# Kernel optimization log

Measured on AMD Instinct MI355X. Metric: run time of the kernel, lower is better.

## Reference

```python
import jax, jax.numpy as jnp
import numpy as np

B, F, E = 16384, 50, 64          # batch, field_size, embedding_size
V, D = 100000, 512               # feature_size, deep_init_size
H1, H2 = 1024, 512               # deep_layers
BN_EPS = 1e-10


def setup_inputs() -> dict:
    key = jax.random.key(0)
    ks = jax.random.split(key, 14)
    g0 = np.sqrt(6.0 / (D + H1))
    g1 = np.sqrt(6.0 / (H1 + H2))
    go = np.sqrt(5.0 / (D + 1))
    return {
        "feat_index": jax.random.randint(ks[0], (B, F), 0, V),
        "feat_value": jax.random.uniform(ks[1], (B, F), dtype=jnp.float32),
        "feature_embeddings": jax.random.normal(ks[2], (V, E), dtype=jnp.float32) * 0.01,
        "product_linear": jax.random.normal(ks[3], (D, F, E), dtype=jnp.float32) * 0.01,
        "product_bias": jax.random.normal(ks[4], (D,), dtype=jnp.float32),
        "product_quadratic_inner": jax.random.normal(ks[5], (D, F), dtype=jnp.float32) * 0.01,
        "layer_0": jax.random.uniform(ks[6], (D, H1), minval=-g0, maxval=g0, dtype=jnp.float32),
        "bias_0": jax.random.uniform(ks[7], (1, H1), minval=-g0, maxval=g0, dtype=jnp.float32),
        "layer_1": jax.random.uniform(ks[8], (H1, H2), minval=-g1, maxval=g1, dtype=jnp.float32),
        "bias_1": jax.random.uniform(ks[9], (1, H2), minval=-g1, maxval=g1, dtype=jnp.float32),
        "bn_scale": jax.random.normal(ks[10], (1,), dtype=jnp.float32) * 0.01,
        "bn_offset": jax.random.normal(ks[11], (1,), dtype=jnp.float32) * 0.01,
        "output_w": jax.random.uniform(ks[12], (H2, 1), minval=-go, maxval=go, dtype=jnp.float32),
        "output_b": jnp.float32(0.01),
    }


def reference(feat_index, feat_value, feature_embeddings, product_linear,
              product_bias, product_quadratic_inner, layer_0, bias_0,
              layer_1, bias_1, bn_scale, bn_offset, output_w, output_b):
    # embedding lookup scaled by feature values: (B, F, E)
    emb = feature_embeddings[feat_index] * feat_value[..., None]
    # linear product signal: sum over field+embed dims for each of D units
    lz = jnp.einsum('bfe,dfe->bd', emb, product_linear)          # (B, D)
    # inner quadratic signal: field-weighted sum then L2 norm over embed dim
    s = jnp.einsum('bfe,df->bde', emb, product_quadratic_inner)  # (B, D, E)
    lp = jnp.sqrt(jnp.sum(s * s, axis=-1))                       # (B, D)
    y = jax.nn.relu(lz + lp + product_bias)
    # dropout omitted (deterministic eval-mode reference)
    for W, bvec in ((layer_0, bias_0), (layer_1, bias_1)):
        y = y @ W + bvec
        m = jnp.mean(y, axis=0)
        v = jnp.var(y, axis=0)
        y = (y - m) * jax.lax.rsqrt(v + BN_EPS) * bn_scale + bn_offset
        y = jax.nn.relu(y)
    out = y @ output_w + output_b
    return jax.nn.sigmoid(out)
```

## Files before the change

kernel.cpp:

```cpp
#include <hip/hip_runtime.h>

typedef unsigned short u16;
typedef __attribute__((ext_vector_type(8))) short bf16x8v;
typedef __attribute__((ext_vector_type(4))) float f32x4v;

#define B_SZ 16384
#define F_SZ 50
#define E_SZ 64
#define D_SZ 512
#define H1_SZ 1024
#define H2_SZ 512
#define KL 3200
#define KG 1280

__device__ __forceinline__ float b2f(u16 u){
  union { unsigned int i; float f; } v; v.i = ((unsigned int)u) << 16; return v.f;
}
__device__ __forceinline__ u16 f2b(float f){
  union { float f; unsigned int i; } v; v.f = f;
  unsigned int r = v.i + 0x7FFFu + ((v.i >> 16) & 1u);
  return (u16)(r >> 16);
}

__device__ __forceinline__ void gload16(const u16* g, u16* lds_base_uniform){
#if __has_builtin(__builtin_amdgcn_global_load_lds)
  __builtin_amdgcn_global_load_lds(
      (const __attribute__((address_space(1))) unsigned int*)g,
      (__attribute__((address_space(3))) unsigned int*)lds_base_uniform,
      16, 0, 0);
#else
  int lane = threadIdx.x & 63;
  *(uint4*)(lds_base_uniform + lane*8) = *(const uint4*)g;
#endif
}

__device__ __forceinline__ void swz(int id, int nblog2, int &x, int &y){
  int xcd = id & 7, j = id >> 3;
  x = j & ((1 << nblog2) - 1);
  y = ((j >> nblog2) << 3) | xcd;
}

__global__ __launch_bounds__(256) void k_front(
    const int* __restrict__ fidx, const float* __restrict__ fval,
    const float* __restrict__ femb, u16* __restrict__ embT,
    u16* __restrict__ Gp,
    const float* __restrict__ Wl, u16* __restrict__ WlT,
    const float* __restrict__ Pq, u16* __restrict__ pqq,
    const float* __restrict__ w0, u16* __restrict__ w0T,
    const float* __restrict__ w1, u16* __restrict__ w1T,
    const float* __restrict__ pb, const float* __restrict__ b0,
    float* __restrict__ cvec)
{
  __shared__ int   sidx[F_SZ];
  __shared__ float sfv[F_SZ];
  __shared__ __align__(16) u16 tile[64*72];
  __shared__ __align__(16) u16 gbuf[KG];
  const int r = blockIdx.x, t = threadIdx.x;
  if (r < 16384){
    const int b = r;
    const int wave = t >> 6, lane = t & 63, quad = lane >> 4, l16 = lane & 15;
    if (t < F_SZ){ sidx[t] = fidx[b*F_SZ+t]; sfv[t] = fval[b*F_SZ+t]; }
    if (t < 5) gbuf[1275+t] = 0;
    __syncthreads();
    #pragma unroll
    for (int i=0;i<4;i++){
      int k4 = (i*256+t)*4;
      if (k4 < F_SZ*E_SZ){
        int f = k4>>6, e = k4&63;
        float4 v = *(const float4*)&femb[(size_t)sidx[f]*E_SZ + e];
        float s = sfv[f];
        tile[f*72+e+0] = f2b(v.x*s);
        tile[f*72+e+1] = f2b(v.y*s);
        tile[f*72+e+2] = f2b(v.z*s);
        tile[f*72+e+3] = f2b(v.w*s);
      }
    }
    __syncthreads();
    u16* orow = embT + (size_t)b*KL;
    #pragma unroll
    for (int i=0;i<2;i++){
      int k8 = (i*256+t)*8;
      if (k8 < F_SZ*E_SZ){
        int f = k8>>6, e0 = k8&63;
        *(uint4*)&orow[k8] = *(const uint4*)&tile[f*72+e0];
      }
    }
    static const int TM[10] = {0,0,0,0,1,1,1,2,2,3};
    static const int TN[10] = {0,1,2,3,1,2,3,2,3,3};
    for (int ti = wave; ti < 10; ti += 4){
      const int tm = TM[ti], tn = TN[ti];
      f32x4v g = {0.f,0.f,0.f,0.f};
      #pragma unroll
      for (int ks=0;ks<2;ks++){
        bf16x8v af = *(const bf16x8v*)&tile[(tm*16+l16)*72 + (ks*4+quad)*8];
        bf16x8v bf = *(const bf16x8v*)&tile[(tn*16+l16)*72 + (ks*4+quad)*8];
        g = __builtin_amdgcn_mfma_f32_16x16x32_bf16(af, bf, g, 0, 0, 0);
      }
      const int gn = tn*16 + l16;
      #pragma unroll
      for (int rr=0;rr<4;rr++){
        const int gm = tm*16 + quad*4 + rr;
        if (gm < F_SZ && gn < F_SZ && gn >= gm)
          gbuf[gm*F_SZ - ((gm*(gm-1))>>1) + (gn-gm)] = f2b(g[rr]);
      }
    }
    __syncthreads();
    if (t < 160)
      *(uint4*)&Gp[(size_t)b*KG + t*8] = *(const uint4*)&gbuf[t*8];
  } else if (r < 16896){
    const int d = r - 16384;
    #pragma unroll
    for (int i=0;i<4;i++){
      int k4 = (i*256+t)*4;
      if (k4 < KL){
        float4 v = *(const float4*)&Wl[(size_t)d*KL + k4];
        u16* o = &WlT[(size_t)d*KL + k4];
        o[0]=f2b(v.x); o[1]=f2b(v.y); o[2]=f2b(v.z); o[3]=f2b(v.w);
      }
    }
  } else if (r < 17408){
    const int d = r - 16896;
    const float* prow = &Pq[d*F_SZ];
    u16* orow = &pqq[(size_t)d*KG];
    int trif = 0;
    for (int f=0; f<F_SZ; f++){
      int len = F_SZ - f;
      if (t < len)
        orow[trif + t] = f2b(prow[f]*prow[f+t]*(t ? 2.f : 1.f));
      trif += len;
    }
    if (t < 5) orow[1275+t] = 0;
  } else if (r < 19456){
    int idx = (r-17408)*256 + t;
    int k = idx & 511, n = idx >> 9;
    w0T[idx] = f2b(w0[(size_t)k*H1_SZ + n]);
  } else if (r < 21504){
    int idx = (r-19456)*256 + t;
    int k = idx & 1023, n = idx >> 10;
    w1T[idx] = f2b(w1[(size_t)k*H2_SZ + n]);
  } else {
    int rr = r - 21504;
    int h = (rr & 3)*256 + t;
    int d0 = (rr >> 2)*64;
    float acc = (d0 == 0) ? b0[h] : 0.f;
    #pragma unroll 8
    for (int d=0; d<64; d++) acc += pb[d0+d]*w0[(size_t)(d0+d)*H1_SZ + h];
    atomicAdd(&cvec[h], acc);
  }
}


__global__ __launch_bounds__(256, 2) void k_prod(
    const u16* __restrict__ Ae,
    const u16* __restrict__ Bw,
    const u16* __restrict__ Ag,
    const u16* __restrict__ Bq,
    const float* __restrict__ pbias,
    u16* __restrict__ y0)
{
  __shared__ __align__(16) u16 As[128*128];
  __shared__ __align__(16) u16 Bs[128*128];
  const int tid  = threadIdx.x;
  const int wave = tid >> 6, lane = tid & 63;
  const int quad = lane >> 4, l16 = lane & 15;
  int bx, by;  swz(blockIdx.x, 2, bx, by);
  const int n0 = bx * 128, m0 = by * 128;
  const int lr4 = lane >> 4;
  const int cb  = lane & 15;
  const int sw  = (l16 & 7);

  f32x4v acc1[2][8], acc2[2][8];
  #pragma unroll
  for (int i=0;i<2;i++)
    #pragma unroll
    for (int j=0;j<8;j++){
      acc1[i][j] = (f32x4v){0.f,0.f,0.f,0.f};
      acc2[i][j] = (f32x4v){0.f,0.f,0.f,0.f};
    }

  auto run = [&](const u16* Ap, const u16* Bp, int K, f32x4v (&acc)[2][8]){
    for (int k0 = 0; k0 < K; k0 += 128){
      __syncthreads();
      #pragma unroll
      for (int c=0;c<8;c++){
        const int r0 = wave*32 + c*4;
        const int row = r0 + lr4;
        gload16(Ap + (size_t)(m0 + row)*K + k0 + ((cb ^ (row & 7)) << 3), As + r0*128);
      }
      #pragma unroll
      for (int c=0;c<8;c++){
        const int r0 = wave*32 + c*4;
        const int row = r0 + lr4;
        gload16(Bp + (size_t)(n0 + row)*K + k0 + ((cb ^ (row & 7)) << 3), Bs + r0*128);
      }
      __syncthreads();
      #pragma unroll
      for (int ks=0; ks<4; ks++){
        bf16x8v af[2], bfr[8];
        #pragma unroll
        for (int mt=0;mt<2;mt++)
          af[mt] = *(const bf16x8v*)&As[(wave*32+mt*16+l16)*128 + (((ks*4+quad) ^ sw))*8];
        #pragma unroll
        for (int nt=0;nt<8;nt++)
          bfr[nt] = *(const bf16x8v*)&Bs[(nt*16+l16)*128 + (((ks*4+quad) ^ sw))*8];
        #pragma unroll
        for (int mt=0;mt<2;mt++)
          #pragma unroll
          for (int nt=0;nt<8;nt++)
            acc[mt][nt] = __builtin_amdgcn_mfma_f32_16x16x32_bf16(af[mt], bfr[nt], acc[mt][nt], 0, 0, 0);
      }
    }
  };

  run(Ae, Bw, KL, acc1);
  run(Ag, Bq, KG, acc2);

  #pragma unroll
  for (int nt=0;nt<8;nt++){
    const int n = n0 + nt*16 + l16;
    const float bv = pbias[n];
    #pragma unroll
    for (int mt=0;mt<2;mt++){
      const int mb = m0 + wave*32 + mt*16 + quad*4;
      #pragma unroll
      for (int r=0;r<4;r++){
        float v = acc1[mt][nt][r] + sqrtf(fmaxf(acc2[mt][nt][r], 0.f)) + bv;
        v = (v > 0.f ? v : 0.f) - bv;
        y0[(size_t)(mb+r)*D_SZ + n] = f2b(v);
      }
    }
  }
}

template<int DO_STATS, int CENTER, typename CT>
__global__ __launch_bounds__(256) void gemm_bt(
    const u16* __restrict__ A, const u16* __restrict__ Bm,
    CT* __restrict__ C, const float* __restrict__ bias,
    float* __restrict__ S1, float* __restrict__ S2,
    int nblog2, int N, int K)
{
  __shared__ __align__(16) u16 As[64*128];
  __shared__ __align__(16) u16 Bs[128*128];
  const int tid  = threadIdx.x;
  const int wave = tid >> 6, lane = tid & 63;
  const int quad = lane >> 4, l16 = lane & 15;
  int bx, by;  swz(blockIdx.x, nblog2, bx, by);
  const int n0 = bx * 128, m0 = by * 64;
  const int wr = wave >> 1, wc = wave & 1;
  const int lr4 = lane >> 4;
  const int cb  = lane & 15;
  const int sw  = (l16 & 7);

  f32x4v acc[2][4];
  #pragma unroll
  for (int i=0;i<2;i++)
    #pragma unroll
    for (int j=0;j<4;j++)
      acc[i][j] = (f32x4v){0.f,0.f,0.f,0.f};

  for (int k0 = 0; k0 < K; k0 += 128){
    __syncthreads();
    #pragma unroll
    for (int c=0;c<4;c++){
      const int r0 = wave*16 + c*4;
      const int row = r0 + lr4;
      gload16(A + (size_t)(m0 + row)*K + k0 + ((cb ^ (row & 7)) << 3), As + r0*128);
    }
    #pragma unroll
    for (int c=0;c<8;c++){
      const int r0 = wave*32 + c*4;
      const int row = r0 + lr4;
      gload16(Bm + (size_t)(n0 + row)*K + k0 + ((cb ^ (row & 7)) << 3), Bs + r0*128);
    }
    __syncthreads();
    #pragma unroll
    for (int ks=0; ks<4; ks++){
      bf16x8v af[2], bfr[4];
      #pragma unroll
      for (int mt=0;mt<2;mt++)
        af[mt] = *(const bf16x8v*)&As[(wr*32+mt*16+l16)*128 + (((ks*4+quad) ^ sw))*8];
      #pragma unroll
      for (int nt=0;nt<4;nt++)
        bfr[nt] = *(const bf16x8v*)&Bs[(wc*64+nt*16+l16)*128 + (((ks*4+quad) ^ sw))*8];
      #pragma unroll
      for (int mt=0;mt<2;mt++)
        #pragma unroll
        for (int nt=0;nt<4;nt++)
          acc[mt][nt] = __builtin_amdgcn_mfma_f32_16x16x32_bf16(af[mt], bfr[nt], acc[mt][nt], 0, 0, 0);
    }
  }

  #pragma unroll
  for (int nt=0;nt<4;nt++){
    const int n = n0 + wc*64 + nt*16 + l16;
    float bv = 0.f;
    if (DO_STATS) bv = bias[n];
    float ls1 = 0.f, ls2 = 0.f;
    #pragma unroll
    for (int mt=0;mt<2;mt++){
      const int mb = m0 + wr*32 + mt*16 + quad*4;
      #pragma unroll
      for (int r=0;r<4;r++){
        float v = acc[mt][nt][r] + bv;
        if constexpr (sizeof(CT) == 2) C[(size_t)(mb+r)*N + n] = f2b(CENTER ? acc[mt][nt][r] : v);
        else                           C[(size_t)(mb+r)*N + n] = v;
        ls1 += v; ls2 += v*v;
      }
    }
    if (DO_STATS){
      ls1 += __shfl_xor(ls1, 16); ls2 += __shfl_xor(ls2, 16);
      ls1 += __shfl_xor(ls1, 32); ls2 += __shfl_xor(ls2, 32);
      if (quad == 0){ atomicAdd(&S1[n], ls1); atomicAdd(&S2[n], ls2); }
    }
  }
}

__global__ __launch_bounds__(256) void k_bnapply(
    const u16* __restrict__ Z, u16* __restrict__ Y,
    const float* __restrict__ S1, const float* __restrict__ S2,
    const float* __restrict__ bnsc, const float* __restrict__ bnof,
    const float* __restrict__ cadd, int nmask)
{
  size_t base = ((size_t)blockIdx.x*256 + threadIdx.x) * 8;
  int n0 = (int)(base & (size_t)nmask);
  const float invB = 1.f / 16384.f;
  const float sc = bnsc[0], of = bnof[0];
  union { uint4 q; u16 s[8]; } z, o;
  z.q = *(const uint4*)&Z[base];
  #pragma unroll
  for (int j=0;j<8;j++){
    int n = n0 + j;
    float m   = S1[n]*invB;
    float var = S2[n]*invB - m*m;
    float a   = sc * rsqrtf(var + 1e-10f);
    float bb  = of - m*a + a*cadd[n];
    float v = b2f(z.s[j]) * a + bb;
    o.s[j] = f2b(v > 0.f ? v : 0.f);
  }
  *(uint4*)&Y[base] = o.q;
}

__global__ __launch_bounds__(256) void k_out(
    const u16* __restrict__ Z2, const float* __restrict__ wvec,
    const float* __restrict__ obp,
    const float* __restrict__ S1, const float* __restrict__ S2,
    const float* __restrict__ bnsc, const float* __restrict__ bnof,
    const float* __restrict__ cadd,
    float* __restrict__ out)
{
  const int wave = threadIdx.x >> 6, lane = threadIdx.x & 63;
  const int b = blockIdx.x*4 + wave;
  const int n0 = lane*8;
  const float invB = 1.f / 16384.f;
  const float sc = bnsc[0], of = bnof[0];
  union { uint4 q; u16 s[8]; } z;
  z.q = *(const uint4*)&Z2[(size_t)b*H2_SZ + n0];
  float4 wa = *(const float4*)&wvec[n0];
  float4 wb = *(const float4*)&wvec[n0+4];
  float wv[8] = {wa.x,wa.y,wa.z,wa.w,wb.x,wb.y,wb.z,wb.w};
  float s = 0.f;
  #pragma unroll
  for (int j=0;j<8;j++){
    int n = n0 + j;
    float m   = S1[n]*invB;
    float var = S2[n]*invB - m*m;
    float a   = sc * rsqrtf(var + 1e-10f);
    float bb  = of - m*a + a*cadd[n];
    float y = b2f(z.s[j]) * a + bb;
    y = y > 0.f ? y : 0.f;
    s += y * wv[j];
  }
  s += __shfl_xor(s,1);  s += __shfl_xor(s,2);  s += __shfl_xor(s,4);
  s += __shfl_xor(s,8);  s += __shfl_xor(s,16); s += __shfl_xor(s,32);
  if (lane == 0){
    float x = s + obp[0];
    out[b] = 1.f / (1.f + expf(-x));
  }
}


extern "C" void kernel_launch(void* const* d_in, const int* in_sizes, int n_in,
                              void* d_out, int out_size, void* d_ws, size_t ws_size,
                              hipStream_t stream)
{
  const int*   fidx  = (const int*)d_in[0];
  const float* fval  = (const float*)d_in[1];
  const float* femb  = (const float*)d_in[2];
  const float* wl    = (const float*)d_in[3];
  const float* pbias = (const float*)d_in[4];
  const float* pq    = (const float*)d_in[5];
  const float* w0    = (const float*)d_in[6];
  const float* b0    = (const float*)d_in[7];
  const float* w1    = (const float*)d_in[8];
  const float* b1    = (const float*)d_in[9];
  const float* bnsc  = (const float*)d_in[10];
  const float* bnof  = (const float*)d_in[11];
  const float* ow    = (const float*)d_in[12];
  const float* ob    = (const float*)d_in[13];
  float* out = (float*)d_out;

  char* ws = (char*)d_ws;
  u16*   embT = (u16*)(ws + 0);
  u16*   z1b  = (u16*)(ws + 0);
  u16*   y1b  = (u16*)(ws + 67108864);
  u16*   z2b  = (u16*)(ws + 100663296);
  u16*   gpb  = (u16*)(ws + 104857600);
  u16*   wlT  = (u16*)(ws + 146800640);
  u16*   pqqb = (u16*)(ws + 150077440);
  u16*   y0b  = (u16*)(ws + 151388160);
  u16*   w0T  = (u16*)(ws + 168165376);
  u16*   w1T  = (u16*)(ws + 169213952);
  float* S1a  = (float*)(ws + 170262528);
  float* S2a  = S1a + 1024;
  float* S1b  = S2a + 1024;
  float* S2b  = S1b + 512;
  float* cvec = S2b + 512;

  hipMemsetAsync((void*)S1a, 0, 16384, stream);

  k_front<<<21536, 256, 0, stream>>>(fidx, fval, femb, embT, gpb,
                                     wl, wlT, pq, pqqb, w0, w0T, w1, w1T,
                                     pbias, b0, cvec);

  k_prod<<<512, 256, 0, stream>>>(embT, wlT, gpb, pqqb, pbias, y0b);

  gemm_bt<1,1,u16><<<2048, 256, 0, stream>>>(y0b, w0T, z1b, cvec, S1a, S2a,
                                             3, H1_SZ, D_SZ);
  k_bnapply<<<8192, 256, 0, stream>>>(z1b, y1b, S1a, S2a, bnsc, bnof, cvec, 1023);

  gemm_bt<1,1,u16><<<1024, 256, 0, stream>>>(y1b, w1T, z2b, b1, S1b, S2b,
                                             2, H2_SZ, H1_SZ);

  k_out<<<4096, 256, 0, stream>>>(z2b, ow, ob, S1b, S2b, bnsc, bnof, b1, out);
}
```

Measured before the change: 326.6 us.

## Fuse first BatchNorm apply and ReLU into second GEMM's A-tile load

Replaces the standalone BN-apply kernel with a tiny per-column finalize kernel that computes scale and shift vectors. The second GEMM then reads the raw first-layer output, applies scale, shift and ReLU while staging the A tile into LDS, and stores it swizzled. This drops one full write and read of the 16384x1024 bf16 intermediate. In exchange the A tile now goes through registers instead of async global-to-LDS loads, which can stall the GEMM main loop.

```diff
diff --git a/kernel.cpp b/kernel.cpp
--- a/kernel.cpp
+++ b/kernel.cpp
@@ -315,29 +315,112 @@
   }
 }
 
-__global__ __launch_bounds__(256) void k_bnapply(
-    const u16* __restrict__ Z, u16* __restrict__ Y,
-    const float* __restrict__ S1, const float* __restrict__ S2,
-    const float* __restrict__ bnsc, const float* __restrict__ bnof,
-    const float* __restrict__ cadd, int nmask)
-{
-  size_t base = ((size_t)blockIdx.x*256 + threadIdx.x) * 8;
-  int n0 = (int)(base & (size_t)nmask);
+__global__ __launch_bounds__(256) void gemm_bn(
+    const u16* __restrict__ Z,
+    const u16* __restrict__ Bm,
+    const float* __restrict__ Aa, const float* __restrict__ Bb,
+    u16* __restrict__ C,
+    const float* __restrict__ bias,
+    float* __restrict__ S1, float* __restrict__ S2)
+{
+  __shared__ __align__(16) u16 As[64*128];
+  __shared__ __align__(16) u16 Bs[128*128];
+  const int tid  = threadIdx.x;
+  const int wave = tid >> 6, lane = tid & 63;
+  const int quad = lane >> 4, l16 = lane & 15;
+  int bx, by;  swz(blockIdx.x, 2, bx, by);
+  const int n0 = bx * 128, m0 = by * 64;
+  const int wr = wave >> 1, wc = wave & 1;
+  const int lr4 = lane >> 4;
+  const int cb  = lane & 15;
+  const int sw  = (l16 & 7);
+
+  f32x4v acc[2][4];
+  #pragma unroll
+  for (int i=0;i<2;i++)
+    #pragma unroll
+    for (int j=0;j<4;j++)
+      acc[i][j] = (f32x4v){0.f,0.f,0.f,0.f};
+
+  for (int k0 = 0; k0 < H1_SZ; k0 += 128){
+    __syncthreads();
+    #pragma unroll
+    for (int c=0;c<4;c++){
+      const int r0 = wave*16 + c*4;
+      const int row = r0 + lr4;
+      const int col = k0 + ((cb ^ (row & 7)) << 3);
+      union { uint4 q; u16 s[8]; } z, o;
+      z.q = *(const uint4*)&Z[(size_t)(m0 + row)*H1_SZ + col];
+      float4 a0 = *(const float4*)&Aa[col];
+      float4 a1 = *(const float4*)&Aa[col+4];
+      float4 b0 = *(const float4*)&Bb[col];
+      float4 b1 = *(const float4*)&Bb[col+4];
+      float av[8] = {a0.x,a0.y,a0.z,a0.w,a1.x,a1.y,a1.z,a1.w};
+      float bv[8] = {b0.x,b0.y,b0.z,b0.w,b1.x,b1.y,b1.z,b1.w};
+      #pragma unroll
+      for (int j=0;j<8;j++){
+        float v = b2f(z.s[j]) * av[j] + bv[j];
+        o.s[j] = f2b(v > 0.f ? v : 0.f);
+      }
+      *(uint4*)&As[row*128 + cb*8] = o.q;
+    }
+    #pragma unroll
+    for (int c=0;c<8;c++){
+      const int r0 = wave*32 + c*4;
+      const int row = r0 + lr4;
+      gload16(Bm + (size_t)(n0 + row)*H1_SZ + k0 + ((cb ^ (row & 7)) << 3), Bs + r0*128);
+    }
+    __syncthreads();
+    #pragma unroll
+    for (int ks=0; ks<4; ks++){
+      bf16x8v af[2], bfr[4];
+      #pragma unroll
+      for (int mt=0;mt<2;mt++)
+        af[mt] = *(const bf16x8v*)&As[(wr*32+mt*16+l16)*128 + (((ks*4+quad) ^ sw))*8];
+      #pragma unroll
+      for (int nt=0;nt<4;nt++)
+        bfr[nt] = *(const bf16x8v*)&Bs[(wc*64+nt*16+l16)*128 + (((ks*4+quad) ^ sw))*8];
+      #pragma unroll
+      for (int mt=0;mt<2;mt++)
+        #pragma unroll
+        for (int nt=0;nt<4;nt++)
+          acc[mt][nt] = __builtin_amdgcn_mfma_f32_16x16x32_bf16(af[mt], bfr[nt], acc[mt][nt], 0, 0, 0);
+    }
+  }
+
+  #pragma unroll
+  for (int nt=0;nt<4;nt++){
+    const int n = n0 + wc*64 + nt*16 + l16;
+    const float bv = bias[n];
+    float ls1 = 0.f, ls2 = 0.f;
+    #pragma unroll
+    for (int mt=0;mt<2;mt++){
+      const int mb = m0 + wr*32 + mt*16 + quad*4;
+      #pragma unroll
+      for (int r=0;r<4;r++){
+        float v = acc[mt][nt][r] + bv;
+        C[(size_t)(mb+r)*H2_SZ + n] = f2b(acc[mt][nt][r]);
+        ls1 += v; ls2 += v*v;
+      }
+    }
+    ls1 += __shfl_xor(ls1, 16); ls2 += __shfl_xor(ls2, 16);
+    ls1 += __shfl_xor(ls1, 32); ls2 += __shfl_xor(ls2, 32);
+    if (quad == 0){ atomicAdd(&S1[n], ls1); atomicAdd(&S2[n], ls2); }
+  }
+}
+
+__global__ void k_bnfin(const float* __restrict__ S1, const float* __restrict__ S2,
+                        const float* __restrict__ bnsc, const float* __restrict__ bnof,
+                        const float* __restrict__ cadd,
+                        float* __restrict__ Aout, float* __restrict__ Bout)
+{
+  int i = blockIdx.x*256 + threadIdx.x;
   const float invB = 1.f / 16384.f;
-  const float sc = bnsc[0], of = bnof[0];
-  union { uint4 q; u16 s[8]; } z, o;
-  z.q = *(const uint4*)&Z[base];
-  #pragma unroll
-  for (int j=0;j<8;j++){
-    int n = n0 + j;
-    float m   = S1[n]*invB;
-    float var = S2[n]*invB - m*m;
-    float a   = sc * rsqrtf(var + 1e-10f);
-    float bb  = of - m*a + a*cadd[n];
-    float v = b2f(z.s[j]) * a + bb;
-    o.s[j] = f2b(v > 0.f ? v : 0.f);
-  }
-  *(uint4*)&Y[base] = o.q;
+  float m   = S1[i]*invB;
+  float var = S2[i]*invB - m*m;
+  float a   = bnsc[0] * rsqrtf(var + 1e-10f);
+  Aout[i] = a;
+  Bout[i] = bnof[0] - m*a + a*cadd[i];
 }
 
 __global__ __launch_bounds__(256) void k_out(
@@ -402,7 +485,6 @@
   char* ws = (char*)d_ws;
   u16*   embT = (u16*)(ws + 0);
   u16*   z1b  = (u16*)(ws + 0);
-  u16*   y1b  = (u16*)(ws + 67108864);
   u16*   z2b  = (u16*)(ws + 100663296);
   u16*   gpb  = (u16*)(ws + 104857600);
   u16*   wlT  = (u16*)(ws + 146800640);
@@ -415,6 +497,8 @@
   float* S1b  = S2a + 1024;
   float* S2b  = S1b + 512;
   float* cvec = S2b + 512;
+  float* A0   = cvec + 1024;
+  float* B0   = A0 + 1024;
 
   hipMemsetAsync((void*)S1a, 0, 16384, stream);
 
@@ -426,10 +510,9 @@
 
   gemm_bt<1,1,u16><<<2048, 256, 0, stream>>>(y0b, w0T, z1b, cvec, S1a, S2a,
                                              3, H1_SZ, D_SZ);
-  k_bnapply<<<8192, 256, 0, stream>>>(z1b, y1b, S1a, S2a, bnsc, bnof, cvec, 1023);
-
-  gemm_bt<1,1,u16><<<1024, 256, 0, stream>>>(y1b, w1T, z2b, b1, S1b, S2b,
-                                             2, H2_SZ, H1_SZ);
+  k_bnfin<<<4, 256, 0, stream>>>(S1a, S2a, bnsc, bnof, cvec, A0, B0);
+
+  gemm_bn<<<1024, 256, 0, stream>>>(z1b, w1T, A0, B0, z2b, b1, S1b, S2b);
 
   k_out<<<4096, 256, 0, stream>>>(z2b, ow, ob, S1b, S2b, bnsc, bnof, b1, out);
 }
```

Measured after the change: 339.0 us. 1.04x slower.
